# Optimization experiments

Hardware: AMD Instinct MI355X
Metric: run time of the kernel (lower is better)

The kernel has to match this reference:

```python
import jax, jax.numpy as jnp
import numpy as np

NUM_HEADS = 16
HEAD_DIM = 64
KERNEL = 13  # odd
DIM = NUM_HEADS * HEAD_DIM
SCALE = HEAD_DIM ** -0.5


def setup_inputs() -> dict:
    key = jax.random.key(0)
    ks = jax.random.split(key, 6)
    B, L = 4, 4096
    return {
        "x": jax.random.normal(ks[0], (B, L, DIM), jnp.float32),
        "w_qkv": jax.random.normal(ks[1], (DIM, 3 * DIM), jnp.float32) * 0.02,
        "b_qkv": jax.random.normal(ks[2], (3 * DIM,), jnp.float32) * 0.02,
        "rpb": jax.random.normal(ks[3], (NUM_HEADS, 2 * KERNEL - 1), jnp.float32) * 0.02,
        "w_proj": jax.random.normal(ks[4], (DIM, DIM), jnp.float32) * 0.02,
        "b_proj": jax.random.normal(ks[5], (DIM,), jnp.float32) * 0.02,
    }


def _na1d(q, k, v, rpb, kernel_size):
    # q,k,v: [B,H,L,D]; rpb: [H, 2K-1]. dilation == 1.
    L = q.shape[2]
    K = kernel_size
    r = K // 2
    i = jnp.arange(L)
    # neighborhood start, clamped so each query sees exactly K keys (NATTEN semantics)
    ni = jnp.clip(i - r, 0, L - K)                    # [L]
    nbr = ni[:, None] + jnp.arange(K)                 # [L,K] key indices
    k_nb = k[:, :, nbr]                               # [B,H,L,K,D]
    attn = jnp.einsum("bhld,bhlkd->bhlk", q, k_nb)   # windowed QK
    # relative-position-bias start index: bias idx = (key_pos - i) + (K-1)
    pi = ni - i + (K - 1)                             # [L]
    bias = rpb[:, pi[:, None] + jnp.arange(K)]        # [H,L,K]
    attn = jax.nn.softmax(attn + bias[None], axis=-1)
    v_nb = v[:, :, nbr]                               # [B,H,L,K,D]
    return jnp.einsum("bhlk,bhlkd->bhld", attn, v_nb)


def reference(x, w_qkv, b_qkv, rpb, w_proj, b_proj):
    B, L, C = x.shape
    qkv = x @ w_qkv + b_qkv                           # [B,L,3C]
    qkv = qkv.reshape(B, L, 3, NUM_HEADS, HEAD_DIM).transpose(2, 0, 3, 1, 4)
    q, k, v = qkv[0] * SCALE, qkv[1], qkv[2]          # [B,H,L,D]
    out = _na1d(q, k, v, rpb, KERNEL)                 # [B,H,L,D]
    out = out.transpose(0, 2, 1, 3).reshape(B, L, C)
    return out @ w_proj + b_proj
```

## Files before the change

kernel.cpp:

```cpp
#include <hip/hip_runtime.h>

typedef __bf16 bf16x8_t __attribute__((ext_vector_type(8)));
typedef float  f32x4_t  __attribute__((ext_vector_type(4)));
typedef float  floatx4  __attribute__((ext_vector_type(4)));
typedef unsigned short ushortx4 __attribute__((ext_vector_type(4)));

__device__ __forceinline__ float bf2f(unsigned short u) {
    union { unsigned int i; float f; } c; c.i = ((unsigned int)u) << 16; return c.f;
}
__device__ __forceinline__ unsigned short f2bf(float f) {
    union { float f; unsigned int i; } c; c.f = f;
    unsigned int u = c.i;
    u += 0x7fffu + ((u >> 16) & 1u);
    return (unsigned short)(u >> 16);
}
__device__ __forceinline__ void unpack8(uint4 u, float* dst, float sc) {
    dst[0] = bf2f((unsigned short)(u.x & 0xffff)) * sc;
    dst[1] = bf2f((unsigned short)(u.x >> 16)) * sc;
    dst[2] = bf2f((unsigned short)(u.y & 0xffff)) * sc;
    dst[3] = bf2f((unsigned short)(u.y >> 16)) * sc;
    dst[4] = bf2f((unsigned short)(u.z & 0xffff)) * sc;
    dst[5] = bf2f((unsigned short)(u.z >> 16)) * sc;
    dst[6] = bf2f((unsigned short)(u.w & 0xffff)) * sc;
    dst[7] = bf2f((unsigned short)(u.w >> 16)) * sc;
}

__device__ __forceinline__ void load_lds16(const unsigned short* g, unsigned short* l) {
    __builtin_amdgcn_global_load_lds(
        (const __attribute__((address_space(1))) unsigned int*)g,
        (__attribute__((address_space(3))) unsigned int*)l, 16, 0, 0);
}

__global__ __launch_bounds__(256) void convert_f32_bf16(
    const float* __restrict__ x, unsigned short* __restrict__ xb)
{
    size_t i = ((size_t)blockIdx.x * 256 + threadIdx.x) * 8;
    floatx4 a = *reinterpret_cast<const floatx4*>(x + i);
    floatx4 b = *reinterpret_cast<const floatx4*>(x + i + 4);
    uint4 o;
    o.x = (unsigned int)f2bf(a.x) | ((unsigned int)f2bf(a.y) << 16);
    o.y = (unsigned int)f2bf(a.z) | ((unsigned int)f2bf(a.w) << 16);
    o.z = (unsigned int)f2bf(b.x) | ((unsigned int)f2bf(b.y) << 16);
    o.w = (unsigned int)f2bf(b.z) | ((unsigned int)f2bf(b.w) << 16);
    *reinterpret_cast<uint4*>(xb + i) = o;
}

__global__ __launch_bounds__(256) void transpose_f32_to_bf16(
    const float* __restrict__ W, unsigned short* __restrict__ Wt,
    int Kdim, int Ndim)
{
    __shared__ float tile[32][33];
    const int n0 = blockIdx.x * 32, k0 = blockIdx.y * 32;
    const int tx = threadIdx.x & 31, ty = threadIdx.x >> 5;
#pragma unroll
    for (int r = 0; r < 4; ++r) {
        int k = ty + r * 8;
        tile[k][tx] = W[(size_t)(k0 + k) * Ndim + n0 + tx];
    }
    __syncthreads();
#pragma unroll
    for (int r = 0; r < 4; ++r) {
        int n = ty + r * 8;
        Wt[(size_t)(n0 + n) * Kdim + k0 + tx] = f2bf(tile[tx][n]);
    }
}

#define TBM 256
#define TBN 256
#define TBK 32

template<bool C_F32>
__global__ __launch_bounds__(512, 2) void gemm_pipe_kernel(
    const unsigned short* __restrict__ A, const unsigned short* __restrict__ Wt,
    const float* __restrict__ bias, void* __restrict__ Cp,
    int N, int K, int lda, int ldc)
{
    __shared__ __align__(16) unsigned short SMEM[8][8192];

    const int tid  = threadIdx.x;
    const int lane = tid & 63;
    const int wid  = tid >> 6;
    const int wm   = wid >> 2;
    const int wn   = wid & 3;
    const int quad = lane >> 4;
    const int lr   = lane & 15;

    const int gx  = gridDim.x;
    const int cpx = (gx * gridDim.y) >> 3;
    const int bid = blockIdx.y * gx + blockIdx.x;
    const int nid = (bid & 7) * cpx + (bid >> 3);
    const int m0 = (nid / gx) * TBM;
    const int n0 = (nid % gx) * TBN;

    const int s_row = tid >> 2;
    const int c_sw  = ((tid & 3) ^ ((tid >> 3) & 3)) * 8;
    const int xq    = (quad ^ ((lr >> 1) & 3)) * 8;
    const int NT    = K >> 5;

    const unsigned short* Ag  = A  + (size_t)(m0 + s_row) * lda + c_sw;
    const unsigned short* Ag2 = Ag + (size_t)128 * lda;
    const unsigned short* Bg  = Wt + (size_t)(n0 + s_row) * K + c_sw;
    const unsigned short* Bg2 = Bg + (size_t)128 * K;

    f32x4_t acc[8][4];
#pragma unroll
    for (int i = 0; i < 8; ++i)
#pragma unroll
        for (int j = 0; j < 4; ++j)
            acc[i][j] = (f32x4_t){0.f, 0.f, 0.f, 0.f};

#pragma unroll
    for (int tt = 0; tt < 3; ++tt) {
        load_lds16(Ag  + tt * TBK, &SMEM[tt][wid * 512]);
        load_lds16(Ag2 + tt * TBK, &SMEM[tt][4096 + wid * 512]);
        load_lds16(Bg  + tt * TBK, &SMEM[4 + tt][wid * 512]);
        load_lds16(Bg2 + tt * TBK, &SMEM[4 + tt][4096 + wid * 512]);
    }
    asm volatile("s_waitcnt vmcnt(8)" ::: "memory");
    __builtin_amdgcn_s_barrier();

    for (int tt = 0; tt < NT; ++tt) {
        const int b = tt & 3;
        const unsigned short* pa = &SMEM[b][0];
        const unsigned short* pb = &SMEM[4 + b][0];
        const bool st = (tt + 3) < NT;
        const int  sb = (tt + 3) & 3;
        const int  ko = (tt + 3) * TBK;

        if (st) {
            load_lds16(Ag  + ko, &SMEM[sb][wid * 512]);
            load_lds16(Ag2 + ko, &SMEM[sb][4096 + wid * 512]);
            load_lds16(Bg  + ko, &SMEM[4 + sb][wid * 512]);
            load_lds16(Bg2 + ko, &SMEM[4 + sb][4096 + wid * 512]);
        }

        bf16x8_t bv[4], av[8];
#pragma unroll
        for (int j = 0; j < 4; ++j)
            bv[j] = *reinterpret_cast<const bf16x8_t*>(pb + (wn * 64 + j * 16 + lr) * TBK + xq);
#pragma unroll
        for (int i = 0; i < 8; ++i)
            av[i] = *reinterpret_cast<const bf16x8_t*>(pa + (wm * 128 + i * 16 + lr) * TBK + xq);

        __builtin_amdgcn_s_setprio(1);
#pragma unroll
        for (int i = 0; i < 8; ++i)
#pragma unroll
            for (int j = 0; j < 4; ++j)
                acc[i][j] = __builtin_amdgcn_mfma_f32_16x16x32_bf16(av[i], bv[j], acc[i][j], 0, 0, 0);
        __builtin_amdgcn_s_setprio(0);

        if (tt < NT - 3)       asm volatile("s_waitcnt vmcnt(8)" ::: "memory");
        else if (tt == NT - 3) asm volatile("s_waitcnt vmcnt(4)" ::: "memory");
        else                   asm volatile("s_waitcnt vmcnt(0)" ::: "memory");
        __builtin_amdgcn_s_barrier();
    }

    if (C_F32) {
#pragma unroll
        for (int j = 0; j < 4; ++j) {
            int col = n0 + wn * 64 + j * 16 + lr;
            float bj = bias[col];
#pragma unroll
            for (int i = 0; i < 8; ++i) {
                int rbase = m0 + wm * 128 + i * 16 + quad * 4;
#pragma unroll
                for (int r = 0; r < 4; ++r) {
                    float v = acc[i][j][r] + bj;
                    ((float*)Cp)[(size_t)(rbase + r) * ldc + col] = v;
                }
            }
        }
    } else {
        unsigned short* ep = &SMEM[wid][0];
#pragma unroll
        for (int j = 0; j < 4; ++j) {
            float bj = bias[n0 + wn * 64 + j * 16 + lr];
#pragma unroll
            for (int i = 0; i < 8; ++i) {
#pragma unroll
                for (int r = 0; r < 4; ++r) {
                    int row = i * 16 + quad * 4 + r;
                    int col = j * 16 + lr;
                    int ch  = (col >> 3) ^ (row & 7);
                    ep[row * 64 + ch * 8 + (col & 7)] = f2bf(acc[i][j][r] + bj);
                }
            }
        }
        unsigned short* Cb = (unsigned short*)Cp;
        const int cch = lane & 7;
#pragma unroll
        for (int s = 0; s < 16; ++s) {
            int row = s * 8 + (lane >> 3);
            int ch  = cch ^ (row & 7);
            uint4 v = *reinterpret_cast<const uint4*>(&ep[row * 64 + ch * 8]);
            *reinterpret_cast<uint4*>(
                Cb + (size_t)(m0 + wm * 128 + row) * ldc + n0 + wn * 64 + cch * 8) = v;
        }
    }
}

#define BM 128
#define BN 128
#define BK 32
#define LDT 40

template<bool A_F32, bool C_F32, bool BT>
__global__ __launch_bounds__(256) void gemm_bias_kernel(
    const void* __restrict__ Ap, const void* __restrict__ Wp,
    const float* __restrict__ bias, void* __restrict__ Cp,
    int N, int K, int lda, int ldc)
{
    __shared__ __align__(16) unsigned short As[BM * LDT];
    __shared__ __align__(16) unsigned short Bs[BN * LDT];

    const int tid  = threadIdx.x;
    const int lane = tid & 63;
    const int wid  = tid >> 6;
    const int wm   = wid >> 1;
    const int wn   = wid & 1;
    const int quad = lane >> 4;
    const int lr   = lane & 15;

    const int m0 = blockIdx.y * BM;
    const int n0 = blockIdx.x * BN;

    f32x4_t acc[4][4];
#pragma unroll
    for (int i = 0; i < 4; ++i)
#pragma unroll
        for (int j = 0; j < 4; ++j)
            acc[i][j] = (f32x4_t){0.f, 0.f, 0.f, 0.f};

    for (int k0 = 0; k0 < K; k0 += BK) {
        if (A_F32) {
            const float* A = (const float*)Ap;
#pragma unroll
            for (int it = 0; it < 4; ++it) {
                int q   = tid + it * 256;
                int row = q >> 3;
                int col = (q & 7) * 4;
                floatx4 f = *reinterpret_cast<const floatx4*>(A + (size_t)(m0 + row) * lda + k0 + col);
                ushortx4 s;
                s.x = f2bf(f.x); s.y = f2bf(f.y); s.z = f2bf(f.z); s.w = f2bf(f.w);
                *reinterpret_cast<ushortx4*>(&As[row * LDT + col]) = s;
            }
        } else {
            const unsigned short* A = (const unsigned short*)Ap;
            int a_row = tid >> 2;
            int a_col = (tid & 3) * 8;
#pragma unroll
            for (int r = 0; r < 2; ++r) {
                int row = a_row + r * 64;
                uint4 u = *reinterpret_cast<const uint4*>(A + (size_t)(m0 + row) * lda + k0 + a_col);
                *reinterpret_cast<uint4*>(&As[row * LDT + a_col]) = u;
            }
        }
        if (BT) {
            const unsigned short* Wt = (const unsigned short*)Wp;
            int b_row = tid >> 2;
            int b_col = (tid & 3) * 8;
#pragma unroll
            for (int r = 0; r < 2; ++r) {
                int n = b_row + r * 64;
                uint4 u = *reinterpret_cast<const uint4*>(Wt + (size_t)(n0 + n) * K + k0 + b_col);
                *reinterpret_cast<uint4*>(&Bs[n * LDT + b_col]) = u;
            }
        } else {
            const float* W = (const float*)Wp;
#pragma unroll
            for (int it = 0; it < 4; ++it) {
                int q  = tid + it * 256;
                int kk = q >> 5;
                int nn = (q & 31) * 4;
                floatx4 f = *reinterpret_cast<const floatx4*>(W + (size_t)(k0 + kk) * N + n0 + nn);
                Bs[(nn + 0) * LDT + kk] = f2bf(f.x);
                Bs[(nn + 1) * LDT + kk] = f2bf(f.y);
                Bs[(nn + 2) * LDT + kk] = f2bf(f.z);
                Bs[(nn + 3) * LDT + kk] = f2bf(f.w);
            }
        }
        __syncthreads();

        bf16x8_t av[4], bv[4];
#pragma unroll
        for (int i = 0; i < 4; ++i)
            av[i] = *reinterpret_cast<const bf16x8_t*>(&As[(wm * 64 + i * 16 + lr) * LDT + quad * 8]);
#pragma unroll
        for (int j = 0; j < 4; ++j)
            bv[j] = *reinterpret_cast<const bf16x8_t*>(&Bs[(wn * 64 + j * 16 + lr) * LDT + quad * 8]);

#pragma unroll
        for (int i = 0; i < 4; ++i)
#pragma unroll
            for (int j = 0; j < 4; ++j)
                acc[i][j] = __builtin_amdgcn_mfma_f32_16x16x32_bf16(av[i], bv[j], acc[i][j], 0, 0, 0);

        __syncthreads();
    }

#pragma unroll
    for (int j = 0; j < 4; ++j) {
        int col = n0 + wn * 64 + j * 16 + lr;
        float bj = bias[col];
#pragma unroll
        for (int i = 0; i < 4; ++i) {
            int rbase = m0 + wm * 64 + i * 16 + quad * 4;
#pragma unroll
            for (int r = 0; r < 4; ++r) {
                float v = acc[i][j][r] + bj;
                size_t idx = (size_t)(rbase + r) * ldc + col;
                if (C_F32) ((float*)Cp)[idx] = v;
                else       ((unsigned short*)Cp)[idx] = f2bf(v);
            }
        }
    }
}

#define NA_L 4096
#define NA_K 13
#define NA_H 16
#define NA_D 64
#define NA_SCALE 0.125f
#define TL  64
#define WIN 76
#define KD  68

__global__ __launch_bounds__(256) void na1d_tiled_kernel(
    unsigned short* qkv, const float* __restrict__ rpb)
{
    __shared__ __align__(16) float ks[WIN * KD];
    __shared__ __align__(16) float vs[WIN * KD];
    __shared__ __align__(16) float qs[TL * KD];
    __shared__ float wgt[TL][NA_K];

    const int bid = blockIdx.x;
    const int h  = bid & 15;
    const int lt = (bid >> 4) & 63;
    const int b  = bid >> 10;
    const int l0 = lt * TL;
    const int rs = l0 - 6;

    const int t = threadIdx.x;
    const size_t rowbase = (size_t)b * NA_L;

    {
        const int qr = t >> 2;
        const int qc = (t & 3) * 16;
        const unsigned short* qsrc = qkv + (rowbase + l0 + qr) * 3072 + h * 64 + qc;
        uint4 q0 = *reinterpret_cast<const uint4*>(qsrc);
        uint4 q1 = *reinterpret_cast<const uint4*>(qsrc + 8);

        const int r0 = t >> 3;
        const int cc = (t & 7) * 8;
        int g0 = rs + r0;      g0 = g0 < 0 ? 0 : (g0 > NA_L - 1 ? NA_L - 1 : g0);
        int g1 = rs + r0 + 32; g1 = g1 < 0 ? 0 : (g1 > NA_L - 1 ? NA_L - 1 : g1);
        const unsigned short* p0 = qkv + (rowbase + g0) * 3072 + 1024 + h * 64 + cc;
        const unsigned short* p1 = qkv + (rowbase + g1) * 3072 + 1024 + h * 64 + cc;
        uint4 k0 = *reinterpret_cast<const uint4*>(p0);
        uint4 v0 = *reinterpret_cast<const uint4*>(p0 + 1024);
        uint4 k1 = *reinterpret_cast<const uint4*>(p1);
        uint4 v1 = *reinterpret_cast<const uint4*>(p1 + 1024);
        uint4 k2, v2;
        if (t < 96) {
            int g2 = rs + r0 + 64; g2 = g2 < 0 ? 0 : (g2 > NA_L - 1 ? NA_L - 1 : g2);
            const unsigned short* p2 = qkv + (rowbase + g2) * 3072 + 1024 + h * 64 + cc;
            k2 = *reinterpret_cast<const uint4*>(p2);
            v2 = *reinterpret_cast<const uint4*>(p2 + 1024);
        }

        unpack8(q0, &qs[qr * KD + qc], NA_SCALE);
        unpack8(q1, &qs[qr * KD + qc + 8], NA_SCALE);
        unpack8(k0, &ks[r0 * KD + cc], 1.f);
        unpack8(v0, &vs[r0 * KD + cc], 1.f);
        unpack8(k1, &ks[(r0 + 32) * KD + cc], 1.f);
        unpack8(v1, &vs[(r0 + 32) * KD + cc], 1.f);
        if (t < 96) {
            unpack8(k2, &ks[(r0 + 64) * KD + cc], 1.f);
            unpack8(v2, &vs[(r0 + 64) * KD + cc], 1.f);
        }
    }
    __syncthreads();

    {
        const int l  = t & 63;
        const int jb = (t >> 6) * 4;
        int ig = l0 + l;
        int ni = ig - 6;
        if (ni < 0) ni = 0;
        if (ni > NA_L - NA_K) ni = NA_L - NA_K;
        int rid = ni - rs;
        int pi  = ni - ig + 12;
        const floatx4* qr = reinterpret_cast<const floatx4*>(&qs[l * KD]);
        const floatx4* k0 = reinterpret_cast<const floatx4*>(&ks[(rid + jb + 0) * KD]);
        const floatx4* k1 = reinterpret_cast<const floatx4*>(&ks[(rid + jb + 1) * KD]);
        const floatx4* k2 = reinterpret_cast<const floatx4*>(&ks[(rid + jb + 2) * KD]);
        const floatx4* k3 = reinterpret_cast<const floatx4*>(&ks[(rid + jb + 3) * KD]);
        floatx4 a0 = {0,0,0,0}, a1 = {0,0,0,0}, a2 = {0,0,0,0}, a3 = {0,0,0,0};
#pragma unroll
        for (int c = 0; c < 16; ++c) {
            floatx4 qv = qr[c];
            a0 += qv * k0[c];
            a1 += qv * k1[c];
            a2 += qv * k2[c];
            a3 += qv * k3[c];
        }
        float s0 = a0.x + a0.y + a0.z + a0.w;
        float s1 = a1.x + a1.y + a1.z + a1.w;
        float s2 = a2.x + a2.y + a2.z + a2.w;
        float s3 = a3.x + a3.y + a3.z + a3.w;
        const float* rp = rpb + h * 25 + pi;
        if (jb + 0 < NA_K) wgt[l][jb + 0] = s0 + rp[jb + 0];
        if (jb + 1 < NA_K) wgt[l][jb + 1] = s1 + rp[jb + 1];
        if (jb + 2 < NA_K) wgt[l][jb + 2] = s2 + rp[jb + 2];
        if (jb + 3 < NA_K) wgt[l][jb + 3] = s3 + rp[jb + 3];
    }
    __syncthreads();

    if (t < TL) {
        float m = -1e30f;
#pragma unroll
        for (int j = 0; j < NA_K; ++j) m = fmaxf(m, wgt[t][j]);
        float sum = 0.f;
#pragma unroll
        for (int j = 0; j < NA_K; ++j) {
            float e = expf(wgt[t][j] - m);
            wgt[t][j] = e;
            sum += e;
        }
        float inv = 1.f / sum;
#pragma unroll
        for (int j = 0; j < NA_K; ++j) wgt[t][j] *= inv;
    }
    __syncthreads();

    {
        const int l  = t & 63;
        const int d0 = (t >> 6) * 16;
        int ig = l0 + l;
        int ni = ig - 6;
        if (ni < 0) ni = 0;
        if (ni > NA_L - NA_K) ni = NA_L - NA_K;
        int rid = ni - rs;
        floatx4 o0 = {0,0,0,0}, o1 = {0,0,0,0}, o2 = {0,0,0,0}, o3 = {0,0,0,0};
#pragma unroll
        for (int j = 0; j < NA_K; ++j) {
            float w = wgt[l][j];
            const floatx4* vr = reinterpret_cast<const floatx4*>(&vs[(rid + j) * KD + d0]);
            o0 += w * vr[0];
            o1 += w * vr[1];
            o2 += w * vr[2];
            o3 += w * vr[3];
        }
        unsigned short* dst = qkv + (rowbase + ig) * 3072 + h * 64 + d0;
        uint4 p0, p1;
        p0.x = (unsigned int)f2bf(o0.x) | ((unsigned int)f2bf(o0.y) << 16);
        p0.y = (unsigned int)f2bf(o0.z) | ((unsigned int)f2bf(o0.w) << 16);
        p0.z = (unsigned int)f2bf(o1.x) | ((unsigned int)f2bf(o1.y) << 16);
        p0.w = (unsigned int)f2bf(o1.z) | ((unsigned int)f2bf(o1.w) << 16);
        p1.x = (unsigned int)f2bf(o2.x) | ((unsigned int)f2bf(o2.y) << 16);
        p1.y = (unsigned int)f2bf(o2.z) | ((unsigned int)f2bf(o2.w) << 16);
        p1.z = (unsigned int)f2bf(o3.x) | ((unsigned int)f2bf(o3.y) << 16);
        p1.w = (unsigned int)f2bf(o3.z) | ((unsigned int)f2bf(o3.w) << 16);
        *reinterpret_cast<uint4*>(dst)     = p0;
        *reinterpret_cast<uint4*>(dst + 8) = p1;
    }
}

extern "C" void kernel_launch(void* const* d_in, const int* in_sizes, int n_in,
                              void* d_out, int out_size, void* d_ws, size_t ws_size,
                              hipStream_t stream)
{
    const float* x      = (const float*)d_in[0];
    const float* w_qkv  = (const float*)d_in[1];
    const float* b_qkv  = (const float*)d_in[2];
    const float* rpb    = (const float*)d_in[3];
    const float* w_proj = (const float*)d_in[4];
    const float* b_proj = (const float*)d_in[5];
    float* out = (float*)d_out;

    const int M  = 4 * 4096;
    const int K  = 1024;
    const int N1 = 3072;
    const int N2 = 1024;

    unsigned short* qkv = (unsigned short*)d_ws;
    unsigned short* Wt1 = qkv + (size_t)M * N1;
    unsigned short* Wt2 = Wt1 + (size_t)N1 * K;
    unsigned short* xb  = Wt2 + (size_t)N2 * K;
    size_t need_mid  = ((size_t)M * N1 + (size_t)N1 * K + (size_t)N2 * K) * 2;
    size_t need_fast = need_mid + (size_t)M * K * 2;

    const int na_grid = 4 * (NA_L / TL) * NA_H;

    if (ws_size >= need_fast) {
        convert_f32_bf16<<<dim3(M * K / (256 * 8)), 256, 0, stream>>>(x, xb);
        transpose_f32_to_bf16<<<dim3(N1 / 32, K / 32), 256, 0, stream>>>(w_qkv, Wt1, K, N1);
        transpose_f32_to_bf16<<<dim3(N2 / 32, K / 32), 256, 0, stream>>>(w_proj, Wt2, K, N2);
        gemm_pipe_kernel<false><<<dim3(N1 / TBN, M / TBM), 512, 0, stream>>>(
            xb, Wt1, b_qkv, qkv, N1, K, K, N1);
        na1d_tiled_kernel<<<dim3(na_grid), 256, 0, stream>>>(qkv, rpb);
        gemm_pipe_kernel<true><<<dim3(N2 / TBN, M / TBM), 512, 0, stream>>>(
            qkv, Wt2, b_proj, out, N2, K, N1, N2);
    } else if (ws_size >= need_mid) {
        transpose_f32_to_bf16<<<dim3(N1 / 32, K / 32), 256, 0, stream>>>(w_qkv, Wt1, K, N1);
        transpose_f32_to_bf16<<<dim3(N2 / 32, K / 32), 256, 0, stream>>>(w_proj, Wt2, K, N2);
        gemm_bias_kernel<true, false, true><<<dim3(N1 / BN, M / BM), 256, 0, stream>>>(
            x, Wt1, b_qkv, qkv, N1, K, K, N1);
        na1d_tiled_kernel<<<dim3(na_grid), 256, 0, stream>>>(qkv, rpb);
        gemm_bias_kernel<false, true, true><<<dim3(N2 / BN, M / BM), 256, 0, stream>>>(
            qkv, Wt2, b_proj, out, N2, K, N1, N2);
    } else {
        gemm_bias_kernel<true, false, false><<<dim3(N1 / BN, M / BM), 256, 0, stream>>>(
            x, w_qkv, b_qkv, qkv, N1, K, K, N1);
        na1d_tiled_kernel<<<dim3(na_grid), 256, 0, stream>>>(qkv, rpb);
        gemm_bias_kernel<false, true, false><<<dim3(N2 / BN, M / BM), 256, 0, stream>>>(
            qkv, w_proj, b_proj, out, N2, K, N1, N2);
    }
}
```

Measured before the change: 366.3 us.

## Keep neighborhood-attention Q/K/V tiles as bf16 in LDS with XOR swizzle

```diff
diff --git a/kernel.cpp b/kernel.cpp
--- a/kernel.cpp
+++ b/kernel.cpp
@@ -14,15 +14,16 @@
     u += 0x7fffu + ((u >> 16) & 1u);
     return (unsigned short)(u >> 16);
 }
-__device__ __forceinline__ void unpack8(uint4 u, float* dst, float sc) {
-    dst[0] = bf2f((unsigned short)(u.x & 0xffff)) * sc;
-    dst[1] = bf2f((unsigned short)(u.x >> 16)) * sc;
-    dst[2] = bf2f((unsigned short)(u.y & 0xffff)) * sc;
-    dst[3] = bf2f((unsigned short)(u.y >> 16)) * sc;
-    dst[4] = bf2f((unsigned short)(u.z & 0xffff)) * sc;
-    dst[5] = bf2f((unsigned short)(u.z >> 16)) * sc;
-    dst[6] = bf2f((unsigned short)(u.w & 0xffff)) * sc;
-    dst[7] = bf2f((unsigned short)(u.w >> 16)) * sc;
+__device__ __forceinline__ void cvt8(uint4 u, floatx4& lo, floatx4& hi) {
+    union { unsigned int i; float f; } c;
+    c.i = u.x << 16;          lo.x = c.f;
+    c.i = u.x & 0xffff0000u;  lo.y = c.f;
+    c.i = u.y << 16;          lo.z = c.f;
+    c.i = u.y & 0xffff0000u;  lo.w = c.f;
+    c.i = u.z << 16;          hi.x = c.f;
+    c.i = u.z & 0xffff0000u;  hi.y = c.f;
+    c.i = u.w << 16;          hi.z = c.f;
+    c.i = u.w & 0xffff0000u;  hi.w = c.f;
 }
 
 __device__ __forceinline__ void load_lds16(const unsigned short* g, unsigned short* l) {
@@ -324,14 +325,13 @@
 #define NA_SCALE 0.125f
 #define TL  64
 #define WIN 76
-#define KD  68
 
 __global__ __launch_bounds__(256) void na1d_tiled_kernel(
     unsigned short* qkv, const float* __restrict__ rpb)
 {
-    __shared__ __align__(16) float ks[WIN * KD];
-    __shared__ __align__(16) float vs[WIN * KD];
-    __shared__ __align__(16) float qs[TL * KD];
+    __shared__ __align__(16) unsigned short ks_b[WIN * 64];
+    __shared__ __align__(16) unsigned short vs_b[WIN * 64];
+    __shared__ __align__(16) unsigned short qs_b[TL * 64];
     __shared__ float wgt[TL][NA_K];
 
     const int bid = blockIdx.x;
@@ -346,17 +346,17 @@
 
     {
         const int qr = t >> 2;
-        const int qc = (t & 3) * 16;
-        const unsigned short* qsrc = qkv + (rowbase + l0 + qr) * 3072 + h * 64 + qc;
+        const int qi = (t & 3) * 2;
+        const unsigned short* qsrc = qkv + (rowbase + l0 + qr) * 3072 + h * 64 + qi * 8;
         uint4 q0 = *reinterpret_cast<const uint4*>(qsrc);
         uint4 q1 = *reinterpret_cast<const uint4*>(qsrc + 8);
 
         const int r0 = t >> 3;
-        const int cc = (t & 7) * 8;
+        const int ci = t & 7;
         int g0 = rs + r0;      g0 = g0 < 0 ? 0 : (g0 > NA_L - 1 ? NA_L - 1 : g0);
         int g1 = rs + r0 + 32; g1 = g1 < 0 ? 0 : (g1 > NA_L - 1 ? NA_L - 1 : g1);
-        const unsigned short* p0 = qkv + (rowbase + g0) * 3072 + 1024 + h * 64 + cc;
-        const unsigned short* p1 = qkv + (rowbase + g1) * 3072 + 1024 + h * 64 + cc;
+        const unsigned short* p0 = qkv + (rowbase + g0) * 3072 + 1024 + h * 64 + ci * 8;
+        const unsigned short* p1 = qkv + (rowbase + g1) * 3072 + 1024 + h * 64 + ci * 8;
         uint4 k0 = *reinterpret_cast<const uint4*>(p0);
         uint4 v0 = *reinterpret_cast<const uint4*>(p0 + 1024);
         uint4 k1 = *reinterpret_cast<const uint4*>(p1);
@@ -364,20 +364,22 @@
         uint4 k2, v2;
         if (t < 96) {
             int g2 = rs + r0 + 64; g2 = g2 < 0 ? 0 : (g2 > NA_L - 1 ? NA_L - 1 : g2);
-            const unsigned short* p2 = qkv + (rowbase + g2) * 3072 + 1024 + h * 64 + cc;
+            const unsigned short* p2 = qkv + (rowbase + g2) * 3072 + 1024 + h * 64 + ci * 8;
             k2 = *reinterpret_cast<const uint4*>(p2);
             v2 = *reinterpret_cast<const uint4*>(p2 + 1024);
         }
 
-        unpack8(q0, &qs[qr * KD + qc], NA_SCALE);
-        unpack8(q1, &qs[qr * KD + qc + 8], NA_SCALE);
-        unpack8(k0, &ks[r0 * KD + cc], 1.f);
-        unpack8(v0, &vs[r0 * KD + cc], 1.f);
-        unpack8(k1, &ks[(r0 + 32) * KD + cc], 1.f);
-        unpack8(v1, &vs[(r0 + 32) * KD + cc], 1.f);
+        const int qk = qr & 7;
+        *reinterpret_cast<uint4*>(qs_b + qr * 64 + (( qi      ^ qk) * 8)) = q0;
+        *reinterpret_cast<uint4*>(qs_b + qr * 64 + (((qi + 1) ^ qk) * 8)) = q1;
+        const int rk = r0 & 7;
+        *reinterpret_cast<uint4*>(ks_b +  r0       * 64 + ((ci ^ rk) * 8)) = k0;
+        *reinterpret_cast<uint4*>(vs_b +  r0       * 64 + ((ci ^ rk) * 8)) = v0;
+        *reinterpret_cast<uint4*>(ks_b + (r0 + 32) * 64 + ((ci ^ rk) * 8)) = k1;
+        *reinterpret_cast<uint4*>(vs_b + (r0 + 32) * 64 + ((ci ^ rk) * 8)) = v1;
         if (t < 96) {
-            unpack8(k2, &ks[(r0 + 64) * KD + cc], 1.f);
-            unpack8(v2, &vs[(r0 + 64) * KD + cc], 1.f);
+            *reinterpret_cast<uint4*>(ks_b + (r0 + 64) * 64 + ((ci ^ rk) * 8)) = k2;
+            *reinterpret_cast<uint4*>(vs_b + (r0 + 64) * 64 + ((ci ^ rk) * 8)) = v2;
         }
     }
     __syncthreads();
@@ -391,24 +393,38 @@
         if (ni > NA_L - NA_K) ni = NA_L - NA_K;
         int rid = ni - rs;
         int pi  = ni - ig + 12;
-        const floatx4* qr = reinterpret_cast<const floatx4*>(&qs[l * KD]);
-        const floatx4* k0 = reinterpret_cast<const floatx4*>(&ks[(rid + jb + 0) * KD]);
-        const floatx4* k1 = reinterpret_cast<const floatx4*>(&ks[(rid + jb + 1) * KD]);
-        const floatx4* k2 = reinterpret_cast<const floatx4*>(&ks[(rid + jb + 2) * KD]);
-        const floatx4* k3 = reinterpret_cast<const floatx4*>(&ks[(rid + jb + 3) * KD]);
+
+        int r0r = rid + jb + 0; if (r0r > WIN - 1) r0r = WIN - 1;
+        int r1r = rid + jb + 1; if (r1r > WIN - 1) r1r = WIN - 1;
+        int r2r = rid + jb + 2; if (r2r > WIN - 1) r2r = WIN - 1;
+        int r3r = rid + jb + 3; if (r3r > WIN - 1) r3r = WIN - 1;
+
+        const unsigned short* qrow = qs_b + l * 64;
+        const unsigned short* k0p  = ks_b + r0r * 64;
+        const unsigned short* k1p  = ks_b + r1r * 64;
+        const unsigned short* k2p  = ks_b + r2r * 64;
+        const unsigned short* k3p  = ks_b + r3r * 64;
+        const int qk = l & 7;
+        const int x0 = r0r & 7, x1 = r1r & 7, x2 = r2r & 7, x3 = r3r & 7;
+
         floatx4 a0 = {0,0,0,0}, a1 = {0,0,0,0}, a2 = {0,0,0,0}, a3 = {0,0,0,0};
 #pragma unroll
-        for (int c = 0; c < 16; ++c) {
-            floatx4 qv = qr[c];
-            a0 += qv * k0[c];
-            a1 += qv * k1[c];
-            a2 += qv * k2[c];
-            a3 += qv * k3[c];
-        }
-        float s0 = a0.x + a0.y + a0.z + a0.w;
-        float s1 = a1.x + a1.y + a1.z + a1.w;
-        float s2 = a2.x + a2.y + a2.z + a2.w;
-        float s3 = a3.x + a3.y + a3.z + a3.w;
+        for (int c = 0; c < 8; ++c) {
+            floatx4 ql, qh, kl, kh;
+            cvt8(*reinterpret_cast<const uint4*>(qrow + ((c ^ qk) * 8)), ql, qh);
+            cvt8(*reinterpret_cast<const uint4*>(k0p + ((c ^ x0) * 8)), kl, kh);
+            a0 += ql * kl; a0 += qh * kh;
+            cvt8(*reinterpret_cast<const uint4*>(k1p + ((c ^ x1) * 8)), kl, kh);
+            a1 += ql * kl; a1 += qh * kh;
+            cvt8(*reinterpret_cast<const uint4*>(k2p + ((c ^ x2) * 8)), kl, kh);
+            a2 += ql * kl; a2 += qh * kh;
+            cvt8(*reinterpret_cast<const uint4*>(k3p + ((c ^ x3) * 8)), kl, kh);
+            a3 += ql * kl; a3 += qh * kh;
+        }
+        float s0 = (a0.x + a0.y + a0.z + a0.w) * NA_SCALE;
+        float s1 = (a1.x + a1.y + a1.z + a1.w) * NA_SCALE;
+        float s2 = (a2.x + a2.y + a2.z + a2.w) * NA_SCALE;
+        float s3 = (a3.x + a3.y + a3.z + a3.w) * NA_SCALE;
         const float* rp = rpb + h * 25 + pi;
         if (jb + 0 < NA_K) wgt[l][jb + 0] = s0 + rp[jb + 0];
         if (jb + 1 < NA_K) wgt[l][jb + 1] = s1 + rp[jb + 1];
@@ -436,7 +452,7 @@
 
     {
         const int l  = t & 63;
-        const int d0 = (t >> 6) * 16;
+        const int wv = t >> 6;
         int ig = l0 + l;
         int ni = ig - 6;
         if (ni < 0) ni = 0;
@@ -446,13 +462,16 @@
 #pragma unroll
         for (int j = 0; j < NA_K; ++j) {
             float w = wgt[l][j];
-            const floatx4* vr = reinterpret_cast<const floatx4*>(&vs[(rid + j) * KD + d0]);
-            o0 += w * vr[0];
-            o1 += w * vr[1];
-            o2 += w * vr[2];
-            o3 += w * vr[3];
-        }
-        unsigned short* dst = qkv + (rowbase + ig) * 3072 + h * 64 + d0;
+            int r = rid + j;
+            int key = r & 7;
+            const unsigned short* vrow = vs_b + r * 64;
+            floatx4 xl, xh;
+            cvt8(*reinterpret_cast<const uint4*>(vrow + (((2 * wv)     ^ key) * 8)), xl, xh);
+            o0 += w * xl; o1 += w * xh;
+            cvt8(*reinterpret_cast<const uint4*>(vrow + (((2 * wv + 1) ^ key) * 8)), xl, xh);
+            o2 += w * xl; o3 += w * xh;
+        }
+        unsigned short* dst = qkv + (rowbase + ig) * 3072 + h * 64 + wv * 16;
         uint4 p0, p1;
         p0.x = (unsigned int)f2bf(o0.x) | ((unsigned int)f2bf(o0.y) << 16);
         p0.y = (unsigned int)f2bf(o0.z) | ((unsigned int)f2bf(o0.w) << 16);
```

Measured after the change: 347.4 us. 1.05x faster.
